# Performance work log

Measured on AMD Instinct MI355X. Metric: run time of the kernel, lower is better.

The kernel has to match this reference:

```python
import jax, jax.numpy as jnp
import numpy as np

B, S_IMG, S_TXT, D, H, HD = 1, 2048, 512, 3072, 24, 128
A_TOK, A_DIM = 4, 1024
S_TOT = S_IMG + S_TXT
EPS = 1e-6
SCALE = 1.0


def _heads(x):
    # [B, S, D] -> [B, H, S, HD]
    return x.reshape(B, -1, H, HD).transpose(0, 2, 1, 3)


def _rms(x, w):
    return x * jax.lax.rsqrt(jnp.mean(x * x, axis=-1, keepdims=True) + EPS) * w


def _rope(x, cos, sin):
    # diffusers apply_rotary_emb, use_real=True, use_real_unbind_dim=-1
    xr = x.reshape(*x.shape[:-1], HD // 2, 2)
    x1, x2 = xr[..., 0], xr[..., 1]
    x_rot = jnp.stack([-x2, x1], axis=-1).reshape(x.shape)
    return x * cos + x_rot * sin


def _sdpa(q, k, v):
    scores = jnp.einsum('bhqd,bhkd->bhqk', q, k) / np.sqrt(HD).astype(np.float32)
    return jnp.einsum('bhqk,bhkd->bhqd', jax.nn.softmax(scores, axis=-1), v)


def setup_inputs() -> dict:
    key = jax.random.key(0)
    ks = jax.random.split(key, 24)
    s = 0.02
    inp = {
        'hidden_states': jax.random.normal(ks[0], (B, S_IMG, D), jnp.float32),
        'encoder_hidden_states': jax.random.normal(ks[1], (B, S_TXT, D), jnp.float32),
        'adapter_embeds': jax.random.normal(ks[2], (B, A_TOK, A_DIM), jnp.float32),
        'freqs_cos': jnp.cos(jax.random.normal(ks[3], (S_TOT, HD), jnp.float32)),
        'freqs_sin': jnp.sin(jax.random.normal(ks[3], (S_TOT, HD), jnp.float32)),
        'Wq': jax.random.normal(ks[4], (D, D), jnp.float32) * s,
        'bq': jnp.zeros((D,), jnp.float32),
        'Wk': jax.random.normal(ks[5], (D, D), jnp.float32) * s,
        'bk': jnp.zeros((D,), jnp.float32),
        'Wv': jax.random.normal(ks[6], (D, D), jnp.float32) * s,
        'bv': jnp.zeros((D,), jnp.float32),
        'norm_q_w': jnp.ones((HD,), jnp.float32),
        'norm_k_w': jnp.ones((HD,), jnp.float32),
        'Wq_add': jax.random.normal(ks[7], (D, D), jnp.float32) * s,
        'bq_add': jnp.zeros((D,), jnp.float32),
        'Wk_add': jax.random.normal(ks[8], (D, D), jnp.float32) * s,
        'bk_add': jnp.zeros((D,), jnp.float32),
        'Wv_add': jax.random.normal(ks[9], (D, D), jnp.float32) * s,
        'bv_add': jnp.zeros((D,), jnp.float32),
        'norm_added_q_w': jnp.ones((HD,), jnp.float32),
        'norm_added_k_w': jnp.ones((HD,), jnp.float32),
        'Wo': jax.random.normal(ks[10], (D, D), jnp.float32) * s,
        'bo': jnp.zeros((D,), jnp.float32),
        'Wo_add': jax.random.normal(ks[11], (D, D), jnp.float32) * s,
        'bo_add': jnp.zeros((D,), jnp.float32),
        'Wk_adapt': jax.random.normal(ks[12], (A_DIM, D), jnp.float32) * s,
        'Wv_adapt': jax.random.normal(ks[13], (A_DIM, D), jnp.float32) * s,
        'block_scaler': jnp.ones((1,), jnp.float32),
    }
    return inp


def reference(hidden_states, encoder_hidden_states, adapter_embeds, freqs_cos, freqs_sin,
              Wq, bq, Wk, bk, Wv, bv, norm_q_w, norm_k_w,
              Wq_add, bq_add, Wk_add, bk_add, Wv_add, bv_add,
              norm_added_q_w, norm_added_k_w, Wo, bo, Wo_add, bo_add,
              Wk_adapt, Wv_adapt, block_scaler):
    # image-token Q/K/V + per-head RMSNorm
    q = _rms(_heads(hidden_states @ Wq + bq), norm_q_w)
    k = _rms(_heads(hidden_states @ Wk + bk), norm_k_w)
    v = _heads(hidden_states @ Wv + bv)
    # text-token Q/K/V + per-head RMSNorm
    eq = _rms(_heads(encoder_hidden_states @ Wq_add + bq_add), norm_added_q_w)
    ek = _rms(_heads(encoder_hidden_states @ Wk_add + bk_add), norm_added_k_w)
    ev = _heads(encoder_hidden_states @ Wv_add + bv_add)
    # joint sequence: [text, image]
    q = jnp.concatenate([eq, q], axis=2)
    k = jnp.concatenate([ek, k], axis=2)
    v = jnp.concatenate([ev, v], axis=2)
    # RoPE on full joint sequence
    q = _rope(q, freqs_cos, freqs_sin)
    k = _rope(k, freqs_cos, freqs_sin)
    # main joint attention
    hs = _sdpa(q, k, v)                                    # [B,H,S_TOT,HD]
    hs = hs.transpose(0, 2, 1, 3).reshape(B, S_TOT, D)
    # adapter cross-attention (vision-direct branch)
    vd_k = _heads(adapter_embeds @ Wk_adapt)               # [B,H,A_TOK,HD]
    vd_v = _heads(adapter_embeds @ Wv_adapt)
    vd = _sdpa(q, vd_k, vd_v)
    vd = vd.transpose(0, 2, 1, 3).reshape(B, S_TOT, D)
    hs = hs + SCALE * (vd * block_scaler)
    # split back and project
    enc_out = hs[:, :S_TXT] @ Wo_add + bo_add
    img_out = hs[:, S_TXT:] @ Wo + bo
    return img_out, enc_out
```

## Files before the change

kernel.cpp:

```cpp
#include <hip/hip_runtime.h>

typedef unsigned short u16;
typedef short s16x8 __attribute__((ext_vector_type(8)));
typedef float f32x4 __attribute__((ext_vector_type(4)));

#define S_TXTC 512
#define S_TOTC 2560
#define DM 3072
#define NH 24
#define HDM 128

__device__ __forceinline__ float b2f(u16 u){ unsigned int i = ((unsigned int)u)<<16; float f; __builtin_memcpy(&f,&i,4); return f; }
__device__ __forceinline__ u16 f2b(float f){ unsigned int i; __builtin_memcpy(&i,&f,4); unsigned int r = i + 0x7FFFu + ((i>>16)&1u); return (u16)(r>>16); }
__device__ __forceinline__ s16x8 pk8(float4 a, float4 b){
  s16x8 r;
  r[0]=(short)f2b(a.x); r[1]=(short)f2b(a.y); r[2]=(short)f2b(a.z); r[3]=(short)f2b(a.w);
  r[4]=(short)f2b(b.x); r[5]=(short)f2b(b.y); r[6]=(short)f2b(b.z); r[7]=(short)f2b(b.w);
  return r;
}
__device__ __forceinline__ void g2l16(const void* g, void* l){
  __builtin_amdgcn_global_load_lds((const __attribute__((address_space(1))) void*)g,
                                   (__attribute__((address_space(3))) void*)l, 16, 0, 0);
}

__global__ __launch_bounds__(256) void fillv(float* __restrict__ p, int n, float v){
  int i = blockIdx.x*256 + threadIdx.x;
  if (i < n) p[i] = v;
}

__global__ __launch_bounds__(256) void cast2(const float* __restrict__ a, const float* __restrict__ b,
                                             u16* __restrict__ dst, int na8, int n8){
  int i = blockIdx.x*256 + threadIdx.x;
  if (i >= n8) return;
  const float* src = (i < na8)? a + (size_t)i*8 : b + (size_t)(i-na8)*8;
  float4 f0 = *(const float4*)src;
  float4 f1 = *(const float4*)(src+4);
  *(s16x8*)(dst + (size_t)i*8) = pk8(f0,f1);
}

__global__ __launch_bounds__(256) void catbias2(const float* __restrict__ b0, const float* __restrict__ b1,
    const float* __restrict__ b2, const float* __restrict__ c0, const float* __restrict__ c1,
    const float* __restrict__ c2, float* __restrict__ dst){
  int i = blockIdx.x*256 + threadIdx.x;
  if (i >= 18432) return;
  int j = (i < 9216)? i : i - 9216;
  const float* s0 = (i<9216)? b0 : c0; const float* s1 = (i<9216)? b1 : c1; const float* s2 = (i<9216)? b2 : c2;
  dst[i] = (j<3072)? s0[j] : (j<6144? s1[j-3072] : s2[j-6144]);
}

__global__ __launch_bounds__(256) void ktrans3(const float* __restrict__ W0, const float* __restrict__ W1,
    const float* __restrict__ W2, u16* __restrict__ D0, u16* __restrict__ D1, u16* __restrict__ D2){
  const float* W = (blockIdx.z==0)? W0 : ((blockIdx.z==1)? W1 : W2);
  u16* Wt = (blockIdx.z==0)? D0 : ((blockIdx.z==1)? D1 : D2);
  __shared__ __align__(16) u16 t[64*72];
  int nt = blockIdx.x*64, kt_ = blockIdx.y*64;
  int tid = threadIdx.x;
  #pragma unroll
  for (int i=0;i<2;i++){
    int q = tid + 256*i;
    int r = q>>3, c8 = (q&7)*8;
    float4 f0 = *(const float4*)(W + (size_t)(kt_+r)*DM + nt + c8);
    float4 f1 = *(const float4*)(W + (size_t)(kt_+r)*DM + nt + c8 + 4);
    *(s16x8*)&t[r*72 + c8] = pk8(f0,f1);
  }
  __syncthreads();
  #pragma unroll
  for (int i=0;i<2;i++){
    int q = tid + 256*i;
    int n = q>>3, k8 = (q&7)*8;
    s16x8 v;
    #pragma unroll
    for (int j=0;j<8;j++) v[j] = (short)t[(k8+j)*72 + n];
    *(s16x8*)(Wt + (size_t)(nt+n)*DM + kt_ + k8) = v;
  }
}

template<int OUT32>
__device__ __forceinline__ void gcore(u16* la, u16* lb,
    const u16* __restrict__ A, const u16* __restrict__ Bt,
    const float* __restrict__ bias, void* __restrict__ Cv,
    int ldc, int rb, int crb, int cb){
  const int K = DM;
  int tid = threadIdx.x, w = tid>>6, l = tid&63, g = l>>4, c16 = l&15;
  int wr = (w>>1)*64, wc = (w&1)*64;
  f32x4 acc[4][4] = {};
  const u16* aL = A  + (size_t)(rb + w*32 + (l>>2))*K + (l&3)*8;
  const u16* bL = Bt + (size_t)(cb + w*32 + (l>>2))*K + (l&3)*8;
  u16* laB = la + w*1024;
  u16* lbB = lb + w*1024;
  for (int ks=0; ks<K; ks+=32){
    g2l16(aL + ks,                laB);
    g2l16(aL + 16*(size_t)K + ks, laB + 512);
    g2l16(bL + ks,                lbB);
    g2l16(bL + 16*(size_t)K + ks, lbB + 512);
    __syncthreads();
    s16x8 af[4], bf[4];
    #pragma unroll
    for (int m=0;m<4;m++) af[m] = *(const s16x8*)&la[(wr + m*16 + c16)*32 + g*8];
    #pragma unroll
    for (int n=0;n<4;n++) bf[n] = *(const s16x8*)&lb[(wc + n*16 + c16)*32 + g*8];
    #pragma unroll
    for (int m=0;m<4;m++)
      #pragma unroll
      for (int n=0;n<4;n++)
        acc[m][n] = __builtin_amdgcn_mfma_f32_16x16x32_bf16(af[m], bf[n], acc[m][n], 0,0,0);
    __syncthreads();
  }
  #pragma unroll
  for (int n=0;n<4;n++){
    int col = cb + wc + n*16 + c16;
    float bv = bias[col];
    #pragma unroll
    for (int m=0;m<4;m++){
      int r0 = crb + wr + m*16 + g*4;
      #pragma unroll
      for (int r=0;r<4;r++){
        float oo = acc[m][n][r] + bv;
        if (OUT32) ((float*)Cv)[(size_t)(r0+r)*ldc + col] = oo;
        else       ((u16*)Cv)[(size_t)(r0+r)*ldc + col] = f2b(oo);
      }
    }
  }
}

__device__ __forceinline__ void xcd_swz(int& bx, int& by){
  int gx = gridDim.x, nwg = gx*gridDim.y;
  int id = blockIdx.y*gx + blockIdx.x;
  int q = nwg>>3;
  int nid = (id&7)*q + (id>>3);
  bx = nid % gx; by = nid / gx;
}

__global__ __launch_bounds__(256) void qkv_gemm(const u16* __restrict__ A, const u16* __restrict__ Bt,
                                                const float* __restrict__ bias, u16* __restrict__ C){
  __shared__ __align__(16) u16 la[4096];
  __shared__ __align__(16) u16 lb[4096];
  int bx, by; xcd_swz(bx, by);
  gcore<0>(la, lb, A, Bt, bias, C, 3*DM, bx*128, bx*128, by*128);
}

__global__ __launch_bounds__(256) void out_gemm(const u16* __restrict__ hsb,
    const u16* __restrict__ woT, const u16* __restrict__ woaT,
    const float* __restrict__ bo, const float* __restrict__ boa, float* __restrict__ out){
  __shared__ __align__(16) u16 la[4096];
  __shared__ __align__(16) u16 lb[4096];
  int bx, by; xcd_swz(bx, by);
  bool txt = (bx < 4);
  int rb = bx*128;
  const u16* Bt = txt? woaT : woT;
  const float* bias = txt? boa : bo;
  float* dst = txt? out + (size_t)2048*DM : out;
  int crb = txt? rb : rb - 512;
  gcore<1>(la, lb, hsb, Bt, bias, dst, DM, rb, crb, by*128);
}

__global__ __launch_bounds__(256) void epi_fused(
    const u16* __restrict__ qkvI, const u16* __restrict__ qkvT,
    const float* __restrict__ nqw, const float* __restrict__ nkw,
    const float* __restrict__ naq, const float* __restrict__ nak,
    const float* __restrict__ fcos, const float* __restrict__ fsin,
    u16* __restrict__ qh, u16* __restrict__ kh, u16* __restrict__ vt){
  __shared__ __align__(16) u16 t[64*136];
  int blk = blockIdx.x;
  if (blk < 30720){
    int wid = blk*4 + (threadIdx.x>>6);
    int lane = threadIdx.x&63;
    int which = wid / (NH*S_TOTC);
    int rem = wid % (NH*S_TOTC);
    int h = rem / S_TOTC, tok = rem % S_TOTC;
    const u16* src = ((tok<S_TXTC)? qkvT + (size_t)tok*(3*DM) : qkvI + (size_t)(tok-S_TXTC)*(3*DM))
                     + which*DM + h*HDM;
    const float* nw = which? ((tok<S_TXTC)? nak : nkw) : ((tok<S_TXTC)? naq : nqw);
    int d = lane*2;
    unsigned int u = *(const unsigned int*)(src + d);
    float x0 = b2f((u16)(u&0xffffu)), x1 = b2f((u16)(u>>16));
    float ss = x0*x0 + x1*x1;
    #pragma unroll
    for (int m=1;m<64;m<<=1) ss += __shfl_xor(ss, m);
    float rr = rsqrtf(ss*(1.f/128.f) + 1e-6f);
    float y0 = x0*rr*nw[d];
    float y1 = x1*rr*nw[d+1];
    float2 cc = *(const float2*)(fcos + (size_t)tok*HDM + d);
    float2 sn = *(const float2*)(fsin + (size_t)tok*HDM + d);
    float sc = which? 1.0f : 0.08838834764831845f;
    float o0 = (y0*cc.x - y1*sn.x)*sc;
    float o1 = (y1*cc.y + y0*sn.y)*sc;
    u16* dst = (which? kh : qh) + ((size_t)h*S_TOTC + tok)*HDM + d;
    *(unsigned int*)dst = (unsigned int)f2b(o0) | ((unsigned int)f2b(o1)<<16);
  } else {
    int bv = blk - 30720;
    int h = bv % NH, tb = bv / NH;
    int tok0 = tb*64, tid = threadIdx.x;
    #pragma unroll
    for (int i=0;i<4;i++){
      int q = tid + 256*i;
      int tr = q>>4, c8 = (q&15)*8;
      int tok = tok0 + tr;
      const u16* src = ((tok<S_TXTC)? qkvT + (size_t)tok*(3*DM) : qkvI + (size_t)(tok-S_TXTC)*(3*DM))
                       + 2*DM + h*HDM;
      *(s16x8*)&t[tr*136 + c8] = *(const s16x8*)(src + c8);
    }
    __syncthreads();
    #pragma unroll
    for (int i=0;i<4;i++){
      int q = tid + 256*i;
      int d = q>>3, j8 = (q&7)*8;
      s16x8 v;
      #pragma unroll
      for (int j=0;j<8;j++) v[j] = (short)t[(j8+j)*136 + d];
      *(s16x8*)(vt + ((size_t)h*HDM + d)*S_TOTC + tok0 + j8) = v;
    }
  }
}

__global__ __launch_bounds__(256) void adapterk(const float* __restrict__ ad, const float* __restrict__ Wk,
        const float* __restrict__ Wv, u16* __restrict__ vdk, u16* __restrict__ vdv){
  int wid = blockIdx.x*4 + (threadIdx.x>>6);
  int lane = threadIdx.x&63;
  int tensor = wid / (4*DM);
  int rem = wid % (4*DM);
  int tok = rem / DM, col = rem % DM;
  const float* Wp = tensor? Wv : Wk;
  float s = 0.f;
  #pragma unroll
  for (int i=0;i<16;i++){
    int k = lane + 64*i;
    s += ad[tok*1024 + k] * Wp[(size_t)k*DM + col];
  }
  #pragma unroll
  for (int m=1;m<64;m<<=1) s += __shfl_xor(s, m);
  if (lane==0){
    int hh = col>>7, d = col&127;
    (tensor? vdv : vdk)[(hh*4+tok)*HDM + d] = f2b(s);
  }
}

__global__ __launch_bounds__(512,2) void attnk(const u16* __restrict__ qh, const u16* __restrict__ kh,
    const u16* __restrict__ vt, const u16* __restrict__ vdk, const u16* __restrict__ vdv,
    const float* __restrict__ bscale, u16* __restrict__ hs){
  __shared__ __align__(16) u16 kts[2][64*128];
  __shared__ __align__(16) u16 vts[2][128*64];
  __shared__ __align__(16) u16 pwb[128*64];
  int h = blockIdx.y, qb = blockIdx.x*128;
  int tid = threadIdx.x, w = tid>>6, l = tid&63, g = l>>4, c16 = l&15;
  int qrow = qb + w*16 + c16;
  int c7 = c16&7;
  s16x8 qf[4];
  #pragma unroll
  for (int kc=0;kc<4;kc++) qf[kc] = *(const s16x8*)(qh + ((size_t)h*S_TOTC + qrow)*HDM + kc*32 + g*8);
  f32x4 acc[8];
  #pragma unroll
  for (int dt=0;dt<8;dt++) acc[dt] = f32x4{0.f,0.f,0.f,0.f};
  float m_[4] = {-3e38f,-3e38f,-3e38f,-3e38f};
  float l_[4] = {0.f,0.f,0.f,0.f};
  const u16* khB = kh + (size_t)h*S_TOTC*HDM;
  const u16* vtB = vt + (size_t)h*HDM*S_TOTC;

  auto STAGE = [&](int buf, int kb){
    #pragma unroll
    for (int c=0;c<2;c++){
      int krow = w*8 + c*4 + (l>>4);
      int kchunk = (l&15) ^ (krow&7);
      g2l16(khB + (size_t)(kb + krow)*HDM + kchunk*8, &kts[buf][w*1024 + c*512]);
      int vrow = w*16 + c*8 + (l>>3);
      int vchunk = (l&7) ^ (vrow&7);
      g2l16(vtB + (size_t)vrow*S_TOTC + kb + vchunk*8, &vts[buf][w*1024 + c*512]);
    }
  };
  auto COMPUTE = [&](int buf){
    f32x4 s[4];
    #pragma unroll
    for (int su=0;su<4;su++) s[su] = f32x4{0.f,0.f,0.f,0.f};
    __builtin_amdgcn_s_setprio(1);
    #pragma unroll
    for (int su=0;su<4;su++)
      #pragma unroll
      for (int kc=0;kc<4;kc++){
        s16x8 kf = *(const s16x8*)&kts[buf][(su*16+c16)*128 + ((kc*4+g) ^ c7)*8];
        s[su] = __builtin_amdgcn_mfma_f32_16x16x32_bf16(qf[kc], kf, s[su], 0,0,0);
      }
    __builtin_amdgcn_s_setprio(0);
    float tm[4];
    #pragma unroll
    for (int r=0;r<4;r++)
      tm[r] = fmaxf(fmaxf(s[0][r],s[1][r]), fmaxf(s[2][r],s[3][r]));
    #pragma unroll
    for (int m=1;m<16;m<<=1)
      #pragma unroll
      for (int r=0;r<4;r++) tm[r] = fmaxf(tm[r], __shfl_xor(tm[r], m));
    bool need = !__all(tm[0]<=m_[0]+8.f && tm[1]<=m_[1]+8.f && tm[2]<=m_[2]+8.f && tm[3]<=m_[3]+8.f);
    if (need){
      float corr[4];
      #pragma unroll
      for (int r=0;r<4;r++){
        float mn = fmaxf(m_[r], tm[r]);
        corr[r] = __expf(m_[r]-mn);
        m_[r] = mn;
        l_[r] *= corr[r];
      }
      #pragma unroll
      for (int dt=0;dt<8;dt++)
        #pragma unroll
        for (int r=0;r<4;r++) acc[dt][r] *= corr[r];
    }
    float rs[4];
    #pragma unroll
    for (int r=0;r<4;r++){
      rs[r] = 0.f;
      #pragma unroll
      for (int su=0;su<4;su++){ s[su][r] = __expf(s[su][r]-m_[r]); rs[r] += s[su][r]; }
    }
    #pragma unroll
    for (int m=1;m<16;m<<=1)
      #pragma unroll
      for (int r=0;r<4;r++) rs[r] += __shfl_xor(rs[r], m);
    #pragma unroll
    for (int r=0;r<4;r++) l_[r] += rs[r];
    #pragma unroll
    for (int su=0;su<4;su++){
      int kslot = su*2 + (c16>>3);
      #pragma unroll
      for (int r=0;r<4;r++){
        int prow = w*16 + g*4 + r;
        pwb[prow*64 + (kslot ^ (prow&7))*8 + c7] = f2b(s[su][r]);
      }
    }
    int prow = w*16 + c16;
    s16x8 pf0 = *(const s16x8*)&pwb[prow*64 + ((0+g) ^ c7)*8];
    s16x8 pf1 = *(const s16x8*)&pwb[prow*64 + ((4+g) ^ c7)*8];
    __builtin_amdgcn_s_setprio(1);
    #pragma unroll
    for (int dt=0;dt<8;dt++){
      int vrow = dt*16 + c16;
      s16x8 vf0 = *(const s16x8*)&vts[buf][vrow*64 + ((0+g) ^ c7)*8];
      acc[dt] = __builtin_amdgcn_mfma_f32_16x16x32_bf16(pf0, vf0, acc[dt], 0,0,0);
      s16x8 vf1 = *(const s16x8*)&vts[buf][vrow*64 + ((4+g) ^ c7)*8];
      acc[dt] = __builtin_amdgcn_mfma_f32_16x16x32_bf16(pf1, vf1, acc[dt], 0,0,0);
    }
    __builtin_amdgcn_s_setprio(0);
  };

  STAGE(0, 0);
  __syncthreads();
  int cur = 0;
  for (int kb=0; kb<S_TOTC; kb+=64){
    if (kb+64 < S_TOTC) STAGE(cur^1, kb+64);
    COMPUTE(cur);
    __syncthreads();
    cur ^= 1;
  }

  if (tid < 64){
    int row = tid>>4, slot = (tid&15) ^ (row&7);
    *(s16x8*)&kts[0][row*128 + slot*8] = *(const s16x8*)(vdk + (h*4+(tid>>4))*HDM + (tid&15)*8);
  } else if (tid < 192){
    int d = tid - 64;
    int sl0 = (d&7)*8;
    #pragma unroll
    for (int key=0;key<4;key++) vts[0][d*64 + sl0 + key] = vdv[(h*4+key)*HDM + d];
  }
  __syncthreads();
  f32x4 s2 = {0.f,0.f,0.f,0.f};
  #pragma unroll
  for (int kc=0;kc<4;kc++){
    s16x8 kf = *(const s16x8*)&kts[0][c16*128 + ((kc*4+g) ^ c7)*8];
    s2 = __builtin_amdgcn_mfma_f32_16x16x32_bf16(qf[kc], kf, s2, 0,0,0);
  }
  bool valid = (c16 < 4);
  float m2[4], l2[4];
  #pragma unroll
  for (int r=0;r<4;r++) m2[r] = valid? s2[r] : -3e38f;
  #pragma unroll
  for (int m=1;m<16;m<<=1)
    #pragma unroll
    for (int r=0;r<4;r++) m2[r] = fmaxf(m2[r], __shfl_xor(m2[r], m));
  #pragma unroll
  for (int r=0;r<4;r++){ float p = valid? __expf(s2[r]-m2[r]) : 0.f; s2[r]=p; l2[r]=p; }
  #pragma unroll
  for (int m=1;m<16;m<<=1)
    #pragma unroll
    for (int r=0;r<4;r++) l2[r] += __shfl_xor(l2[r], m);
  #pragma unroll
  for (int r=0;r<4;r++){
    int prow = w*16 + g*4 + r;
    int s0 = (c16>>3) ^ (prow&7);
    int s1 = (2 + (c16>>3)) ^ (prow&7);
    pwb[prow*64 + s0*8 + c7] = f2b(s2[r]);
    pwb[prow*64 + s1*8 + c7] = (u16)0;
  }
  int prow2 = w*16 + c16;
  s16x8 pf2 = *(const s16x8*)&pwb[prow2*64 + (g ^ c7)*8];
  f32x4 a2[8];
  #pragma unroll
  for (int dt=0;dt<8;dt++) a2[dt] = f32x4{0.f,0.f,0.f,0.f};
  #pragma unroll
  for (int dt=0;dt<8;dt++){
    int vrow = dt*16 + c16;
    s16x8 vf = *(const s16x8*)&vts[0][vrow*64 + (g ^ c7)*8];
    a2[dt] = __builtin_amdgcn_mfma_f32_16x16x32_bf16(pf2, vf, a2[dt], 0,0,0);
  }
  float sb = bscale[0];
  float rl[4], rl2[4];
  #pragma unroll
  for (int r=0;r<4;r++){ rl[r] = 1.f/l_[r]; rl2[r] = sb/l2[r]; }
  #pragma unroll
  for (int dt=0;dt<8;dt++)
    #pragma unroll
    for (int r=0;r<4;r++){
      int tok = qb + w*16 + g*4 + r;
      int col = h*HDM + dt*16 + c16;
      hs[(size_t)tok*DM + col] = f2b(acc[dt][r]*rl[r] + a2[dt][r]*rl2[r]);
    }
}

extern "C" void kernel_launch(void* const* d_in, const int* in_sizes, int n_in,
                              void* d_out, int out_size, void* d_ws, size_t ws_size,
                              hipStream_t stream){
  static const int expect[28] = {
    6291456, 1572864, 4096, 327680, 327680,
    9437184, 3072, 9437184, 3072, 9437184, 3072, 128, 128,
    9437184, 3072, 9437184, 3072, 9437184, 3072, 128, 128,
    9437184, 3072, 9437184, 3072, 3145728, 3145728, 1 };
  bool ok = (n_in == 28);
  if (ok) for (int i=0;i<28;i++) if (in_sizes[i] != expect[i]) { ok = false; break; }
  if (!ok){ fillv<<<(out_size+255)/256,256,0,stream>>>((float*)d_out, out_size, 7.0f); return; }
  if (ws_size < 119611392ull){ fillv<<<(out_size+255)/256,256,0,stream>>>((float*)d_out, out_size, 9.0f); return; }

  const float* hidden = (const float*)d_in[0];
  const float* enc    = (const float*)d_in[1];
  const float* adapt  = (const float*)d_in[2];
  const float* fcos   = (const float*)d_in[3];
  const float* fsin   = (const float*)d_in[4];
  const float* Wq  = (const float*)d_in[5];  const float* bq  = (const float*)d_in[6];
  const float* Wk  = (const float*)d_in[7];  const float* bk  = (const float*)d_in[8];
  const float* Wv  = (const float*)d_in[9];  const float* bv  = (const float*)d_in[10];
  const float* nqw = (const float*)d_in[11]; const float* nkw = (const float*)d_in[12];
  const float* Wqa = (const float*)d_in[13]; const float* bqa = (const float*)d_in[14];
  const float* Wka = (const float*)d_in[15]; const float* bka = (const float*)d_in[16];
  const float* Wva = (const float*)d_in[17]; const float* bva = (const float*)d_in[18];
  const float* naq = (const float*)d_in[19]; const float* nak = (const float*)d_in[20];
  const float* Wo  = (const float*)d_in[21]; const float* bo  = (const float*)d_in[22];
  const float* Woa = (const float*)d_in[23]; const float* boa = (const float*)d_in[24];
  const float* Wkad = (const float*)d_in[25]; const float* Wvad = (const float*)d_in[26];
  const float* bsc  = (const float*)d_in[27];
  float* out = (float*)d_out;

  char* ws = (char*)d_ws;
  u16* wt3   = (u16*)(ws);
  u16* kh    = (u16*)(ws);
  u16* vth   = (u16*)(ws + 15728640);
  u16* vdk   = (u16*)(ws + 31457280);
  u16* vdv   = (u16*)(ws + 31481856);
  u16* woaT  = (u16*)(ws + 33554432);
  u16* hbf   = (u16*)(ws + 56623104);
  u16* ebf   = (u16*)(ws + 69206016);
  u16* qh    = (u16*)(ws + 56623104);
  u16* qkvI  = (u16*)(ws + 72351744);
  u16* hsb   = (u16*)(ws + 72351744);
  u16* woT   = (u16*)(ws + 88080384);
  u16* qkvT  = (u16*)(ws + 110100480);
  float* biasA = (float*)(ws + 119537664);
  float* biasB = (float*)(ws + 119574528);

  cast2<<<3840,256,0,stream>>>(hidden, enc, hbf, 786432, 983040);
  catbias2<<<72,256,0,stream>>>(bq,bk,bv, bqa,bka,bva, biasA);
  ktrans3<<<dim3(48,48,3),256,0,stream>>>(Wq, Wk, Wv, wt3, wt3 + (size_t)DM*DM, wt3 + (size_t)2*DM*DM);
  qkv_gemm<<<dim3(16,72),256,0,stream>>>(hbf, wt3, biasA, qkvI);
  ktrans3<<<dim3(48,48,3),256,0,stream>>>(Wqa, Wka, Wva, wt3, wt3 + (size_t)DM*DM, wt3 + (size_t)2*DM*DM);
  qkv_gemm<<<dim3(4,72),256,0,stream>>>(ebf, wt3, biasB, qkvT);
  epi_fused<<<31680,256,0,stream>>>(qkvI, qkvT, nqw,nkw,naq,nak, fcos,fsin, qh, kh, vth);
  adapterk<<<6144,256,0,stream>>>(adapt, Wkad, Wvad, vdk, vdv);
  attnk<<<dim3(20,24),512,0,stream>>>(qh, kh, vth, vdk, vdv, bsc, hsb);
  ktrans3<<<dim3(48,48,2),256,0,stream>>>(Wo, Woa, Woa, woT, woaT, woaT);
  out_gemm<<<dim3(20,24),256,0,stream>>>(hsb, woT, woaT, bo, boa, out);
}
```

Before: 681.2 us.

## Fuse small launches, use exp2 softmax and hardware bf16 conversion

Merges the cast and bias-concat kernels into one launch, and folds the adapter K/V projection into the epilogue kernel, removing two launches. The softmax switches from __expf to exp2f by folding log2(e) into the Q scale, with the rescale threshold adjusted to match. Float-to-bf16 conversion now uses the HIP intrinsic instead of manual rounding. The text-token GEMM now reads its input from the contiguous cast buffer at an offset. The fused kernels add branching, and the bf16 intrinsic's rounding or NaN handling may differ slightly.

```diff
diff --git a/kernel.cpp b/kernel.cpp
--- a/kernel.cpp
+++ b/kernel.cpp
@@ -1,4 +1,5 @@
 #include <hip/hip_runtime.h>
+#include <hip/hip_bf16.h>
 
 typedef unsigned short u16;
 typedef short s16x8 __attribute__((ext_vector_type(8)));
@@ -11,11 +12,20 @@
 #define HDM 128
 
 __device__ __forceinline__ float b2f(u16 u){ unsigned int i = ((unsigned int)u)<<16; float f; __builtin_memcpy(&f,&i,4); return f; }
-__device__ __forceinline__ u16 f2b(float f){ unsigned int i; __builtin_memcpy(&i,&f,4); unsigned int r = i + 0x7FFFu + ((i>>16)&1u); return (u16)(r>>16); }
+__device__ __forceinline__ u16 f2b(float f){
+  __hip_bfloat16 h = __float2bfloat16(f);
+  u16 r; __builtin_memcpy(&r, &h, 2); return r;
+}
+__device__ __forceinline__ unsigned int pk2(float lo, float hi){
+  return (unsigned int)f2b(lo) | ((unsigned int)f2b(hi)<<16);
+}
 __device__ __forceinline__ s16x8 pk8(float4 a, float4 b){
   s16x8 r;
-  r[0]=(short)f2b(a.x); r[1]=(short)f2b(a.y); r[2]=(short)f2b(a.z); r[3]=(short)f2b(a.w);
-  r[4]=(short)f2b(b.x); r[5]=(short)f2b(b.y); r[6]=(short)f2b(b.z); r[7]=(short)f2b(b.w);
+  unsigned int u0 = pk2(a.x,a.y), u1 = pk2(a.z,a.w), u2 = pk2(b.x,b.y), u3 = pk2(b.z,b.w);
+  __builtin_memcpy(&r, &u0, 4);
+  __builtin_memcpy(((char*)&r)+4, &u1, 4);
+  __builtin_memcpy(((char*)&r)+8, &u2, 4);
+  __builtin_memcpy(((char*)&r)+12, &u3, 4);
   return r;
 }
 __device__ __forceinline__ void g2l16(const void* g, void* l){
@@ -28,24 +38,26 @@
   if (i < n) p[i] = v;
 }
 
-__global__ __launch_bounds__(256) void cast2(const float* __restrict__ a, const float* __restrict__ b,
-                                             u16* __restrict__ dst, int na8, int n8){
-  int i = blockIdx.x*256 + threadIdx.x;
-  if (i >= n8) return;
-  const float* src = (i < na8)? a + (size_t)i*8 : b + (size_t)(i-na8)*8;
-  float4 f0 = *(const float4*)src;
-  float4 f1 = *(const float4*)(src+4);
-  *(s16x8*)(dst + (size_t)i*8) = pk8(f0,f1);
-}
-
-__global__ __launch_bounds__(256) void catbias2(const float* __restrict__ b0, const float* __restrict__ b1,
-    const float* __restrict__ b2, const float* __restrict__ c0, const float* __restrict__ c1,
-    const float* __restrict__ c2, float* __restrict__ dst){
-  int i = blockIdx.x*256 + threadIdx.x;
-  if (i >= 18432) return;
-  int j = (i < 9216)? i : i - 9216;
-  const float* s0 = (i<9216)? b0 : c0; const float* s1 = (i<9216)? b1 : c1; const float* s2 = (i<9216)? b2 : c2;
-  dst[i] = (j<3072)? s0[j] : (j<6144? s1[j-3072] : s2[j-6144]);
+__global__ __launch_bounds__(256) void castbias(const float* __restrict__ a, const float* __restrict__ b,
+    u16* __restrict__ dst, int na8, int n8,
+    const float* __restrict__ b0, const float* __restrict__ b1, const float* __restrict__ b2,
+    const float* __restrict__ c0, const float* __restrict__ c1, const float* __restrict__ c2,
+    float* __restrict__ bdst){
+  int blk = blockIdx.x;
+  if (blk < 3840){
+    int i = blk*256 + threadIdx.x;
+    if (i >= n8) return;
+    const float* src = (i < na8)? a + (size_t)i*8 : b + (size_t)(i-na8)*8;
+    float4 f0 = *(const float4*)src;
+    float4 f1 = *(const float4*)(src+4);
+    *(s16x8*)(dst + (size_t)i*8) = pk8(f0,f1);
+  } else {
+    int i = (blk-3840)*256 + threadIdx.x;
+    if (i >= 18432) return;
+    int j = (i < 9216)? i : i - 9216;
+    const float* s0 = (i<9216)? b0 : c0; const float* s1 = (i<9216)? b1 : c1; const float* s2 = (i<9216)? b2 : c2;
+    bdst[i] = (j<3072)? s0[j] : (j<6144? s1[j-3072] : s2[j-6144]);
+  }
 }
 
 __global__ __launch_bounds__(256) void ktrans3(const float* __restrict__ W0, const float* __restrict__ W1,
@@ -159,7 +171,9 @@
     const float* __restrict__ nqw, const float* __restrict__ nkw,
     const float* __restrict__ naq, const float* __restrict__ nak,
     const float* __restrict__ fcos, const float* __restrict__ fsin,
-    u16* __restrict__ qh, u16* __restrict__ kh, u16* __restrict__ vt){
+    u16* __restrict__ qh, u16* __restrict__ kh, u16* __restrict__ vt,
+    const float* __restrict__ ad, const float* __restrict__ Wkad, const float* __restrict__ Wvad,
+    u16* __restrict__ vdk, u16* __restrict__ vdv){
   __shared__ __align__(16) u16 t[64*136];
   int blk = blockIdx.x;
   if (blk < 30720){
@@ -182,12 +196,12 @@
     float y1 = x1*rr*nw[d+1];
     float2 cc = *(const float2*)(fcos + (size_t)tok*HDM + d);
     float2 sn = *(const float2*)(fsin + (size_t)tok*HDM + d);
-    float sc = which? 1.0f : 0.08838834764831845f;
+    float sc = which? 1.0f : 0.1275174436f;
     float o0 = (y0*cc.x - y1*sn.x)*sc;
     float o1 = (y1*cc.y + y0*sn.y)*sc;
     u16* dst = (which? kh : qh) + ((size_t)h*S_TOTC + tok)*HDM + d;
-    *(unsigned int*)dst = (unsigned int)f2b(o0) | ((unsigned int)f2b(o1)<<16);
-  } else {
+    *(unsigned int*)dst = pk2(o0, o1);
+  } else if (blk < 31680){
     int bv = blk - 30720;
     int h = bv % NH, tb = bv / NH;
     int tok0 = tb*64, tid = threadIdx.x;
@@ -210,28 +224,25 @@
       for (int j=0;j<8;j++) v[j] = (short)t[(j8+j)*136 + d];
       *(s16x8*)(vt + ((size_t)h*HDM + d)*S_TOTC + tok0 + j8) = v;
     }
-  }
-}
-
-__global__ __launch_bounds__(256) void adapterk(const float* __restrict__ ad, const float* __restrict__ Wk,
-        const float* __restrict__ Wv, u16* __restrict__ vdk, u16* __restrict__ vdv){
-  int wid = blockIdx.x*4 + (threadIdx.x>>6);
-  int lane = threadIdx.x&63;
-  int tensor = wid / (4*DM);
-  int rem = wid % (4*DM);
-  int tok = rem / DM, col = rem % DM;
-  const float* Wp = tensor? Wv : Wk;
-  float s = 0.f;
-  #pragma unroll
-  for (int i=0;i<16;i++){
-    int k = lane + 64*i;
-    s += ad[tok*1024 + k] * Wp[(size_t)k*DM + col];
-  }
-  #pragma unroll
-  for (int m=1;m<64;m<<=1) s += __shfl_xor(s, m);
-  if (lane==0){
-    int hh = col>>7, d = col&127;
-    (tensor? vdv : vdk)[(hh*4+tok)*HDM + d] = f2b(s);
+  } else {
+    int wid = (blk-31680)*4 + (threadIdx.x>>6);
+    int lane = threadIdx.x&63;
+    int tensor = wid / (4*DM);
+    int rem = wid % (4*DM);
+    int tok = rem / DM, col = rem % DM;
+    const float* Wp = tensor? Wvad : Wkad;
+    float s = 0.f;
+    #pragma unroll
+    for (int i=0;i<16;i++){
+      int k = lane + 64*i;
+      s += ad[tok*1024 + k] * Wp[(size_t)k*DM + col];
+    }
+    #pragma unroll
+    for (int m=1;m<64;m<<=1) s += __shfl_xor(s, m);
+    if (lane==0){
+      int hh = col>>7, d = col&127;
+      (tensor? vdv : vdk)[(hh*4+tok)*HDM + d] = f2b(s);
+    }
   }
 }
 
@@ -288,13 +299,14 @@
     for (int m=1;m<16;m<<=1)
       #pragma unroll
       for (int r=0;r<4;r++) tm[r] = fmaxf(tm[r], __shfl_xor(tm[r], m));
-    bool need = !__all(tm[0]<=m_[0]+8.f && tm[1]<=m_[1]+8.f && tm[2]<=m_[2]+8.f && tm[3]<=m_[3]+8.f);
+    bool need = !__all(tm[0]<=m_[0]+11.5415603f && tm[1]<=m_[1]+11.5415603f &&
+                       tm[2]<=m_[2]+11.5415603f && tm[3]<=m_[3]+11.5415603f);
     if (need){
       float corr[4];
       #pragma unroll
       for (int r=0;r<4;r++){
         float mn = fmaxf(m_[r], tm[r]);
-        corr[r] = __expf(m_[r]-mn);
+        corr[r] = exp2f(m_[r]-mn);
         m_[r] = mn;
         l_[r] *= corr[r];
       }
@@ -308,7 +320,7 @@
     for (int r=0;r<4;r++){
       rs[r] = 0.f;
       #pragma unroll
-      for (int su=0;su<4;su++){ s[su][r] = __expf(s[su][r]-m_[r]); rs[r] += s[su][r]; }
+      for (int su=0;su<4;su++){ s[su][r] = exp2f(s[su][r]-m_[r]); rs[r] += s[su][r]; }
     }
     #pragma unroll
     for (int m=1;m<16;m<<=1)
@@ -375,7 +387,7 @@
     #pragma unroll
     for (int r=0;r<4;r++) m2[r] = fmaxf(m2[r], __shfl_xor(m2[r], m));
   #pragma unroll
-  for (int r=0;r<4;r++){ float p = valid? __expf(s2[r]-m2[r]) : 0.f; s2[r]=p; l2[r]=p; }
+  for (int r=0;r<4;r++){ float p = valid? exp2f(s2[r]-m2[r]) : 0.f; s2[r]=p; l2[r]=p; }
   #pragma unroll
   for (int m=1;m<16;m<<=1)
     #pragma unroll
@@ -453,7 +465,6 @@
   u16* vdv   = (u16*)(ws + 31481856);
   u16* woaT  = (u16*)(ws + 33554432);
   u16* hbf   = (u16*)(ws + 56623104);
-  u16* ebf   = (u16*)(ws + 69206016);
   u16* qh    = (u16*)(ws + 56623104);
   u16* qkvI  = (u16*)(ws + 72351744);
   u16* hsb   = (u16*)(ws + 72351744);
@@ -462,14 +473,14 @@
   float* biasA = (float*)(ws + 119537664);
   float* biasB = (float*)(ws + 119574528);
 
-  cast2<<<3840,256,0,stream>>>(hidden, enc, hbf, 786432, 983040);
-  catbias2<<<72,256,0,stream>>>(bq,bk,bv, bqa,bka,bva, biasA);
+  castbias<<<3912,256,0,stream>>>(hidden, enc, hbf, 786432, 983040,
+                                  bq,bk,bv, bqa,bka,bva, biasA);
   ktrans3<<<dim3(48,48,3),256,0,stream>>>(Wq, Wk, Wv, wt3, wt3 + (size_t)DM*DM, wt3 + (size_t)2*DM*DM);
   qkv_gemm<<<dim3(16,72),256,0,stream>>>(hbf, wt3, biasA, qkvI);
   ktrans3<<<dim3(48,48,3),256,0,stream>>>(Wqa, Wka, Wva, wt3, wt3 + (size_t)DM*DM, wt3 + (size_t)2*DM*DM);
-  qkv_gemm<<<dim3(4,72),256,0,stream>>>(ebf, wt3, biasB, qkvT);
-  epi_fused<<<31680,256,0,stream>>>(qkvI, qkvT, nqw,nkw,naq,nak, fcos,fsin, qh, kh, vth);
-  adapterk<<<6144,256,0,stream>>>(adapt, Wkad, Wvad, vdk, vdv);
+  qkv_gemm<<<dim3(4,72),256,0,stream>>>(hbf + (size_t)2048*DM, wt3, biasB, qkvT);
+  epi_fused<<<37824,256,0,stream>>>(qkvI, qkvT, nqw,nkw,naq,nak, fcos,fsin, qh, kh, vth,
+                                    adapt, Wkad, Wvad, vdk, vdv);
   attnk<<<dim3(20,24),512,0,stream>>>(qh, kh, vth, vdk, vdv, bsc, hsb);
   ktrans3<<<dim3(48,48,2),256,0,stream>>>(Wo, Woa, Woa, woT, woaT, woaT);
   out_gemm<<<dim3(20,24),256,0,stream>>>(hsb, woT, woaT, bo, boa, out);
```

Measured after the change: 708.1 us. 3.9% more time.
